# Performance work log

Measured on AMD Instinct MI355X. Metric: run time of the kernel, lower is better.

## Reference

```python
import jax, jax.numpy as jnp
import numpy as np

TAU = 2.0
V_TH = 0.5
SG_ALPHA = 4.0
BN_EPS = 1e-5
NUM_HEADS = 8

@jax.custom_vjp
def spike_fn(x):
    return (x >= 0.0).astype(x.dtype)

def _spike_fwd(x):
    return (x >= 0.0).astype(x.dtype), x

def _spike_bwd(x, g):
    s = jax.nn.sigmoid(SG_ALPHA * x)
    return (g * SG_ALPHA * s * (1.0 - s),)

spike_fn.defvjp(_spike_fwd, _spike_bwd)

def lif(x_seq):
    """Multi-step LIF (spikingjelly step_mode='m'): x_seq [T, ...] -> spikes [T, ...].
    v <- v + (x - v)/tau ; spike = H(v - v_th) ; hard reset with detached spike."""
    def step(v, x):
        v = v + (x - v) / TAU
        s = spike_fn(v - V_TH)
        v = v * (1.0 - jax.lax.stop_gradient(s))
        return v, s
    _, s_seq = jax.lax.scan(step, jnp.zeros_like(x_seq[0]), x_seq)
    return s_seq

def conv1x1(x, w, b=None):
    # x: [T,B,C,H,W], w: [Cout,Cin]
    y = jnp.einsum('tbchw,oc->tbohw', x, w)
    if b is not None:
        y = y + b[:, None, None]
    return y

def bn(x, p):
    # eval-mode BatchNorm2d; p = [gamma, beta, mean, var] each [C]
    g, b, m, v = p[0], p[1], p[2], p[3]
    scale = g / jnp.sqrt(v + BN_EPS)
    return x * scale[:, None, None] + (b - m * scale)[:, None, None]

def setup_inputs() -> dict:
    key = jax.random.key(0)
    ks = jax.random.split(key, 20)
    T, B, C, H, W = 4, 8, 512, 32, 32
    Ch = 2048
    def bn_params(k, c):
        kk = jax.random.split(k, 4)
        gamma = jax.random.uniform(kk[0], (c,), jnp.float32, 0.5, 1.5)
        beta = jax.random.normal(kk[1], (c,), jnp.float32) * 0.1
        mean = jax.random.normal(kk[2], (c,), jnp.float32) * 0.1
        var = jax.random.uniform(kk[3], (c,), jnp.float32, 0.5, 1.5)
        return jnp.stack([gamma, beta, mean, var])
    s = 1.0 / np.sqrt(C)
    sh = 1.0 / np.sqrt(Ch)
    return {
        'x': jax.random.normal(ks[0], (T, B, C, H, W), jnp.float32),
        'q_w': jax.random.normal(ks[1], (C, C), jnp.float32) * s,
        'q_bn': bn_params(ks[2], C),
        'k_w': jax.random.normal(ks[3], (C, C), jnp.float32) * s,
        'k_bn': bn_params(ks[4], C),
        'v_w': jax.random.normal(ks[5], (C, C), jnp.float32) * s,
        'v_bn': bn_params(ks[6], C),
        'th_w': jax.random.normal(ks[7], (NUM_HEADS, NUM_HEADS), jnp.float32) / np.sqrt(NUM_HEADS),
        'proj_w': jax.random.normal(ks[8], (C, C), jnp.float32) * s,
        'proj_b': jax.random.normal(ks[9], (C,), jnp.float32) * 0.02,
        'proj_bn': bn_params(ks[10], C),
        'fc1_w': jax.random.normal(ks[11], (Ch, C), jnp.float32) * s,
        'fc1_b': jax.random.normal(ks[12], (Ch,), jnp.float32) * 0.02,
        'fc1_bn': bn_params(ks[13], Ch),
        'fc2_w': jax.random.normal(ks[14], (C, Ch), jnp.float32) * sh,
        'fc2_b': jax.random.normal(ks[15], (C,), jnp.float32) * 0.02,
        'fc2_bn': bn_params(ks[16], C),
    }

def reference(x, q_w, q_bn, k_w, k_bn, v_w, v_bn, th_w, proj_w, proj_b, proj_bn,
              fc1_w, fc1_b, fc1_bn, fc2_w, fc2_b, fc2_bn):
    T, B, C, H, W = x.shape
    N = H * W
    h = NUM_HEADS
    d = C // h

    # ---- MS_SSA_Conv ----
    identity = x
    xs = lif(x)  # shortcut_lif

    def to_heads(t):  # [T,B,C,H,W] -> [T,B,h,N,d]
        t = t.reshape(T, B, C, N).transpose(0, 1, 3, 2)        # [T,B,N,C]
        return t.reshape(T, B, N, h, d).transpose(0, 1, 3, 2, 4)

    q = to_heads(lif(bn(conv1x1(xs, q_w), q_bn)))
    k = to_heads(lif(bn(conv1x1(xs, k_w), k_bn)))
    v = to_heads(lif(bn(conv1x1(xs, v_w), v_bn)))

    kv = (k * v).sum(axis=3, keepdims=True)                    # [T,B,h,1,d]
    kv = jnp.einsum('tbhod,gh->tbgod', kv, th_w)               # talking heads (Conv1d k=1)
    kv = lif(kv)                                               # talking_heads_lif

    x_att = q * kv                                             # [T,B,h,N,d]
    x_att = x_att.transpose(0, 1, 2, 4, 3).reshape(T, B, C, H, W)
    x_out = bn(conv1x1(x_att, proj_w, proj_b), proj_bn) + identity

    # ---- MS_MLP_Conv (res=False since hidden != in) ----
    identity2 = x_out
    hdn = lif(bn(conv1x1(x_out, fc1_w, fc1_b), fc1_bn))
    out = lif(bn(conv1x1(hdn, fc2_w, fc2_b), fc2_bn)) + identity2
    return out
```

## Files before the change

### kernel.cpp

```cpp
#include <hip/hip_runtime.h>

typedef unsigned char u8;
typedef unsigned int u32;

#define T_STEPS 4
#define B_SZ 8
#define C_IN 512
#define CH 2048
#define N_SP 1024
#define S_C ((size_t)B_SZ * C_IN * N_SP)

__global__ __launch_bounds__(256) void lif_x_kernel(const float* __restrict__ in,
                                                    u8* __restrict__ out)
{
    size_t i = (size_t)blockIdx.x * 256 + threadIdx.x;
    float v = 0.0f;
    #pragma unroll
    for (int t = 0; t < T_STEPS; ++t) {
        float x = in[(size_t)t * S_C + i];
        v += (x - v) * 0.5f;
        u8 s = (v >= 0.5f) ? 1 : 0;
        out[(size_t)t * S_C + i] = s;
        v = s ? 0.0f : v;
    }
}

template<int MODE, int BSRC, bool BIAS, int K, int CO, int NSEL>
__global__ __launch_bounds__(256) void mm(
    const float* __restrict__ W0, const float* __restrict__ W1, const float* __restrict__ W2,
    const void* __restrict__ Xv,
    const float* __restrict__ bn0, const float* __restrict__ bn1, const float* __restrict__ bn2,
    const float* __restrict__ bias,
    const float* __restrict__ kvsf,
    const float* __restrict__ res,
    void* Y0, void* Y1, void* Y2)
{
    constexpr int NB_CO = CO / 64;
    constexpr int NB_N = N_SP / 64;
    constexpr int KT = K / 16;

    __shared__ float As[16][68];
    __shared__ float Xs[4][16][68];

    const int bid = blockIdx.x;
    const int nblk = bid % NB_N;
    int slot = bid / NB_N;
    const int cb = slot % NB_CO; slot /= NB_CO;
    const int sel = (NSEL > 1) ? (slot % NSEL) : 0;
    const int b   = (NSEL > 1) ? (slot / NSEL) : slot;

    const float* W   = (NSEL == 1 || sel == 0) ? W0  : (sel == 1 ? W1  : W2);
    const float* bnp = (NSEL == 1 || sel == 0) ? bn0 : (sel == 1 ? bn1 : bn2);
    void* Yv         = (NSEL == 1 || sel == 0) ? Y0  : (sel == 1 ? Y1  : Y2);

    const int coBase = cb * 64;
    const int n0blk = nblk * 64;
    const int tid = threadIdx.x;
    const int tx = tid & 15, ty = tid >> 4;

    const int wr = tid >> 2;
    const int wk4 = (tid & 3) * 4;

    float scale[4], shift[4];
    #pragma unroll
    for (int i = 0; i < 4; ++i) {
        const int co = coBase + ty * 4 + i;
        const float g = bnp[co], be = bnp[CO + co];
        const float mn = bnp[2 * CO + co], vr = bnp[3 * CO + co];
        scale[i] = g / sqrtf(vr + 1e-5f);
        shift[i] = be - mn * scale[i];
        if (BIAS) shift[i] += bias[co] * scale[i];
    }

    float acc[4][4][4];
    #pragma unroll
    for (int t = 0; t < 4; ++t)
        #pragma unroll
        for (int i = 0; i < 4; ++i)
            #pragma unroll
            for (int j = 0; j < 4; ++j) acc[t][i][j] = 0.0f;

    float4 wreg;
    u32 xu[4];
    float mreg[4];
    float4 xf[4];

    auto prefetch = [&](int kt) {
        wreg = *reinterpret_cast<const float4*>(
            W + (size_t)(coBase + wr) * K + kt * 16 + wk4);
        #pragma unroll
        for (int t = 0; t < 4; ++t) {
            const int tb = t * B_SZ + b;
            if constexpr (BSRC <= 1) {
                xu[t] = *reinterpret_cast<const u32*>(
                    (const u8*)Xv + (size_t)tb * K * N_SP
                    + (size_t)(kt * 16 + ty) * N_SP + n0blk + tx * 4);
                if constexpr (BSRC == 1)
                    mreg[t] = kvsf[(size_t)tb * K + kt * 16 + ty];
            } else {
                xf[t] = *reinterpret_cast<const float4*>(
                    (const float*)Xv + (size_t)tb * K * N_SP
                    + (size_t)(kt * 16 + ty) * N_SP + n0blk + tx * 4);
            }
        }
    };

    prefetch(0);

    for (int kt = 0; kt < KT; ++kt) {
        __syncthreads();
        As[wk4 + 0][wr] = wreg.x;
        As[wk4 + 1][wr] = wreg.y;
        As[wk4 + 2][wr] = wreg.z;
        As[wk4 + 3][wr] = wreg.w;
        #pragma unroll
        for (int t = 0; t < 4; ++t) {
            float4 s0;
            if constexpr (BSRC <= 1) {
                s0.x = (float)( xu[t]        & 0xFFu);
                s0.y = (float)((xu[t] >> 8 ) & 0xFFu);
                s0.z = (float)((xu[t] >> 16) & 0xFFu);
                s0.w = (float)( xu[t] >> 24        );
                if constexpr (BSRC == 1) {
                    s0.x *= mreg[t]; s0.y *= mreg[t];
                    s0.z *= mreg[t]; s0.w *= mreg[t];
                }
            } else {
                s0 = xf[t];
            }
            *reinterpret_cast<float4*>(&Xs[t][ty][tx * 4]) = s0;
        }
        __syncthreads();
        if (kt + 1 < KT) prefetch(kt + 1);

        #pragma unroll
        for (int kk = 0; kk < 16; ++kk) {
            float4 av = *reinterpret_cast<const float4*>(&As[kk][ty * 4]);
            float wa[4] = {av.x, av.y, av.z, av.w};
            #pragma unroll
            for (int t = 0; t < 4; ++t) {
                float4 xv = *reinterpret_cast<const float4*>(&Xs[t][kk][tx * 4]);
                float xw[4] = {xv.x, xv.y, xv.z, xv.w};
                #pragma unroll
                for (int i = 0; i < 4; ++i)
                    #pragma unroll
                    for (int j = 0; j < 4; ++j)
                        acc[t][i][j] += wa[i] * xw[j];
            }
        }
    }

    #pragma unroll
    for (int i = 0; i < 4; ++i) {
        const int co = coBase + ty * 4 + i;
        float v[4] = {0.0f, 0.0f, 0.0f, 0.0f};
        #pragma unroll
        for (int t = 0; t < 4; ++t) {
            const int tb = t * B_SZ + b;
            const size_t off = ((size_t)tb * CO + co) * N_SP + n0blk + tx * 4;
            if constexpr (MODE == 0) {
                u32 pk = 0;
                #pragma unroll
                for (int e = 0; e < 4; ++e) {
                    const float y = acc[t][i][e] * scale[i] + shift[i];
                    v[e] += (y - v[e]) * 0.5f;
                    const u32 s = (v[e] >= 0.5f) ? 1u : 0u;
                    v[e] = s ? 0.0f : v[e];
                    pk |= s << (8 * e);
                }
                *reinterpret_cast<u32*>((u8*)Yv + off) = pk;
            } else if constexpr (MODE == 1) {
                float4 r0 = *reinterpret_cast<const float4*>(res + off);
                float rr[4] = {r0.x, r0.y, r0.z, r0.w};
                float o[4];
                #pragma unroll
                for (int e = 0; e < 4; ++e)
                    o[e] = acc[t][i][e] * scale[i] + shift[i] + rr[e];
                float4 s0 = {o[0], o[1], o[2], o[3]};
                *reinterpret_cast<float4*>((float*)Yv + off) = s0;
            } else {
                float* op = (float*)Yv + off;
                float4 r0 = *reinterpret_cast<const float4*>(op);
                float rr[4] = {r0.x, r0.y, r0.z, r0.w};
                float o[4];
                #pragma unroll
                for (int e = 0; e < 4; ++e) {
                    const float y = acc[t][i][e] * scale[i] + shift[i];
                    v[e] += (y - v[e]) * 0.5f;
                    const u32 s = (v[e] >= 0.5f) ? 1u : 0u;
                    v[e] = s ? 0.0f : v[e];
                    o[e] = rr[e] + (s ? 1.0f : 0.0f);
                }
                float4 s0 = {o[0], o[1], o[2], o[3]};
                *reinterpret_cast<float4*>(op) = s0;
            }
        }
    }
}

__global__ __launch_bounds__(256) void kv_reduce(const u8* __restrict__ ks,
                                                 const u8* __restrict__ vs,
                                                 float* __restrict__ kv)
{
    const int row = blockIdx.x * 4 + (threadIdx.x >> 6);
    const int lane = threadIdx.x & 63;
    const u8* kp = ks + (size_t)row * N_SP;
    const u8* vp = vs + (size_t)row * N_SP;
    int acc = 0;
    #pragma unroll
    for (int n = 0; n < N_SP; n += 256) {
        uchar4 a = *reinterpret_cast<const uchar4*>(kp + n + lane * 4);
        uchar4 c = *reinterpret_cast<const uchar4*>(vp + n + lane * 4);
        acc += (a.x & c.x) + (a.y & c.y) + (a.z & c.z) + (a.w & c.w);
    }
    #pragma unroll
    for (int off = 32; off; off >>= 1) acc += __shfl_down(acc, off, 64);
    if (lane == 0) kv[row] = (float)acc;
}

__global__ __launch_bounds__(256) void th_lif(const float* __restrict__ kvraw,
                                              const float* __restrict__ th,
                                              float* __restrict__ kvs)
{
    const int i = blockIdx.x * 256 + threadIdx.x;
    const int b = i >> 9;
    const int c = i & 511;
    const int g = c >> 6;
    const int dd = c & 63;
    float v = 0.0f;
    #pragma unroll
    for (int t = 0; t < T_STEPS; ++t) {
        const float* base = kvraw + ((size_t)t * B_SZ + b) * C_IN;
        float x = 0.0f;
        #pragma unroll
        for (int hh = 0; hh < 8; ++hh)
            x += base[hh * 64 + dd] * th[g * 8 + hh];
        v += (x - v) * 0.5f;
        const float s = (v >= 0.5f) ? 1.0f : 0.0f;
        kvs[((size_t)t * B_SZ + b) * C_IN + c] = s;
        v = (s != 0.0f) ? 0.0f : v;
    }
}

extern "C" void kernel_launch(void* const* d_in, const int* in_sizes, int n_in,
                              void* d_out, int out_size, void* d_ws, size_t ws_size,
                              hipStream_t stream)
{
    const float* x       = (const float*)d_in[0];
    const float* q_w     = (const float*)d_in[1];
    const float* q_bn    = (const float*)d_in[2];
    const float* k_w     = (const float*)d_in[3];
    const float* k_bn    = (const float*)d_in[4];
    const float* v_w     = (const float*)d_in[5];
    const float* v_bn    = (const float*)d_in[6];
    const float* th_w    = (const float*)d_in[7];
    const float* proj_w  = (const float*)d_in[8];
    const float* proj_b  = (const float*)d_in[9];
    const float* proj_bn = (const float*)d_in[10];
    const float* fc1_w   = (const float*)d_in[11];
    const float* fc1_b   = (const float*)d_in[12];
    const float* fc1_bn  = (const float*)d_in[13];
    const float* fc2_w   = (const float*)d_in[14];
    const float* fc2_b   = (const float*)d_in[15];
    const float* fc2_bn  = (const float*)d_in[16];
    float* out = (float*)d_out;

    u8* ws = (u8*)d_ws;
    const size_t SLOT = (size_t)T_STEPS * S_C;
    u8* xs = ws;
    u8* qs = ws + SLOT;
    u8* ks = ws + 2 * SLOT;
    u8* vs = ws + 3 * SLOT;
    float* kvraw = (float*)(ws + 4 * SLOT);
    float* kvsf  = kvraw + (size_t)T_STEPS * B_SZ * C_IN;
    u8* hdn = ws;

    lif_x_kernel<<<(int)(S_C / 256), 256, 0, stream>>>(x, xs);

    mm<0, 0, false, 512, 512, 3><<<3072, 256, 0, stream>>>(
        q_w, k_w, v_w, xs, q_bn, k_bn, v_bn, nullptr, nullptr, nullptr, qs, ks, vs);

    kv_reduce<<<(T_STEPS * B_SZ * C_IN) / 4, 256, 0, stream>>>(ks, vs, kvraw);
    th_lif<<<(B_SZ * C_IN) / 256, 256, 0, stream>>>(kvraw, th_w, kvsf);

    mm<1, 1, true, 512, 512, 1><<<1024, 256, 0, stream>>>(
        proj_w, nullptr, nullptr, qs, proj_bn, nullptr, nullptr, proj_b, kvsf, x,
        out, nullptr, nullptr);

    mm<0, 2, true, 512, 2048, 1><<<4096, 256, 0, stream>>>(
        fc1_w, nullptr, nullptr, out, fc1_bn, nullptr, nullptr, fc1_b, nullptr, nullptr,
        hdn, nullptr, nullptr);

    mm<2, 0, true, 2048, 512, 1><<<1024, 256, 0, stream>>>(
        fc2_w, nullptr, nullptr, hdn, fc2_bn, nullptr, nullptr, fc2_b, nullptr, nullptr,
        out, nullptr, nullptr);
}
```

Measured before the change: 2.390 ms.

## Parameterize matmul tile height by wave count and reorder block indexing

```diff
diff --git a/kernel.cpp b/kernel.cpp
--- a/kernel.cpp
+++ b/kernel.cpp
@@ -25,8 +25,8 @@
     }
 }
 
-template<int MODE, int BSRC, bool BIAS, int K, int CO, int NSEL>
-__global__ __launch_bounds__(256) void mm(
+template<int NW, int MODE, int BSRC, bool BIAS, int K, int CO, int NSEL>
+__global__ __launch_bounds__(NW * 64) void mm(
     const float* __restrict__ W0, const float* __restrict__ W1, const float* __restrict__ W2,
     const void* __restrict__ Xv,
     const float* __restrict__ bn0, const float* __restrict__ bn1, const float* __restrict__ bn2,
@@ -35,25 +35,29 @@
     const float* __restrict__ res,
     void* Y0, void* Y1, void* Y2)
 {
-    constexpr int NB_CO = CO / 64;
-    constexpr int NB_N = N_SP / 64;
+    constexpr int BM = NW * 16;
+    constexpr int NB_CB = CO / BM;
+    constexpr int CBTOT = NB_CB * NSEL;
     constexpr int KT = K / 16;
-
-    __shared__ float As[16][68];
+    constexpr int TYN = NW * 4;
+    constexpr int HX = 16 / TYN;
+
+    __shared__ float As[16][BM + 4];
     __shared__ float Xs[4][16][68];
 
     const int bid = blockIdx.x;
-    const int nblk = bid % NB_N;
-    int slot = bid / NB_N;
-    const int cb = slot % NB_CO; slot /= NB_CO;
-    const int sel = (NSEL > 1) ? (slot % NSEL) : 0;
-    const int b   = (NSEL > 1) ? (slot / NSEL) : slot;
+    const int cbsel = bid % CBTOT;
+    const int rr = bid / CBTOT;
+    const int nblk = rr % 16;
+    const int b = rr / 16;
+    const int cb = (NSEL > 1) ? (cbsel % NB_CB) : cbsel;
+    const int sel = (NSEL > 1) ? (cbsel / NB_CB) : 0;
 
     const float* W   = (NSEL == 1 || sel == 0) ? W0  : (sel == 1 ? W1  : W2);
     const float* bnp = (NSEL == 1 || sel == 0) ? bn0 : (sel == 1 ? bn1 : bn2);
     void* Yv         = (NSEL == 1 || sel == 0) ? Y0  : (sel == 1 ? Y1  : Y2);
 
-    const int coBase = cb * 64;
+    const int coBase = cb * BM;
     const int n0blk = nblk * 64;
     const int tid = threadIdx.x;
     const int tx = tid & 15, ty = tid >> 4;
@@ -81,9 +85,9 @@
             for (int j = 0; j < 4; ++j) acc[t][i][j] = 0.0f;
 
     float4 wreg;
-    u32 xu[4];
-    float mreg[4];
-    float4 xf[4];
+    u32 xu[4][HX];
+    float mreg[4][HX];
+    float4 xf[4][HX];
 
     auto prefetch = [&](int kt) {
         wreg = *reinterpret_cast<const float4*>(
@@ -91,16 +95,20 @@
         #pragma unroll
         for (int t = 0; t < 4; ++t) {
             const int tb = t * B_SZ + b;
-            if constexpr (BSRC <= 1) {
-                xu[t] = *reinterpret_cast<const u32*>(
-                    (const u8*)Xv + (size_t)tb * K * N_SP
-                    + (size_t)(kt * 16 + ty) * N_SP + n0blk + tx * 4);
-                if constexpr (BSRC == 1)
-                    mreg[t] = kvsf[(size_t)tb * K + kt * 16 + ty];
-            } else {
-                xf[t] = *reinterpret_cast<const float4*>(
-                    (const float*)Xv + (size_t)tb * K * N_SP
-                    + (size_t)(kt * 16 + ty) * N_SP + n0blk + tx * 4);
+            #pragma unroll
+            for (int h = 0; h < HX; ++h) {
+                const int row = kt * 16 + ty + TYN * h;
+                if constexpr (BSRC <= 1) {
+                    xu[t][h] = *reinterpret_cast<const u32*>(
+                        (const u8*)Xv + (size_t)tb * K * N_SP
+                        + (size_t)row * N_SP + n0blk + tx * 4);
+                    if constexpr (BSRC == 1)
+                        mreg[t][h] = kvsf[(size_t)tb * K + row];
+                } else {
+                    xf[t][h] = *reinterpret_cast<const float4*>(
+                        (const float*)Xv + (size_t)tb * K * N_SP
+                        + (size_t)row * N_SP + n0blk + tx * 4);
+                }
             }
         }
     };
@@ -115,20 +123,23 @@
         As[wk4 + 3][wr] = wreg.w;
         #pragma unroll
         for (int t = 0; t < 4; ++t) {
-            float4 s0;
-            if constexpr (BSRC <= 1) {
-                s0.x = (float)( xu[t]        & 0xFFu);
-                s0.y = (float)((xu[t] >> 8 ) & 0xFFu);
-                s0.z = (float)((xu[t] >> 16) & 0xFFu);
-                s0.w = (float)( xu[t] >> 24        );
-                if constexpr (BSRC == 1) {
-                    s0.x *= mreg[t]; s0.y *= mreg[t];
-                    s0.z *= mreg[t]; s0.w *= mreg[t];
+            #pragma unroll
+            for (int h = 0; h < HX; ++h) {
+                float4 s0;
+                if constexpr (BSRC <= 1) {
+                    s0.x = (float)( xu[t][h]        & 0xFFu);
+                    s0.y = (float)((xu[t][h] >> 8 ) & 0xFFu);
+                    s0.z = (float)((xu[t][h] >> 16) & 0xFFu);
+                    s0.w = (float)( xu[t][h] >> 24        );
+                    if constexpr (BSRC == 1) {
+                        s0.x *= mreg[t][h]; s0.y *= mreg[t][h];
+                        s0.z *= mreg[t][h]; s0.w *= mreg[t][h];
+                    }
+                } else {
+                    s0 = xf[t][h];
                 }
-            } else {
-                s0 = xf[t];
+                *reinterpret_cast<float4*>(&Xs[t][ty + TYN * h][tx * 4]) = s0;
             }
-            *reinterpret_cast<float4*>(&Xs[t][ty][tx * 4]) = s0;
         }
         __syncthreads();
         if (kt + 1 < KT) prefetch(kt + 1);
@@ -171,17 +182,17 @@
                 *reinterpret_cast<u32*>((u8*)Yv + off) = pk;
             } else if constexpr (MODE == 1) {
                 float4 r0 = *reinterpret_cast<const float4*>(res + off);
-                float rr[4] = {r0.x, r0.y, r0.z, r0.w};
+                float rr2[4] = {r0.x, r0.y, r0.z, r0.w};
                 float o[4];
                 #pragma unroll
                 for (int e = 0; e < 4; ++e)
-                    o[e] = acc[t][i][e] * scale[i] + shift[i] + rr[e];
+                    o[e] = acc[t][i][e] * scale[i] + shift[i] + rr2[e];
                 float4 s0 = {o[0], o[1], o[2], o[3]};
                 *reinterpret_cast<float4*>((float*)Yv + off) = s0;
             } else {
                 float* op = (float*)Yv + off;
                 float4 r0 = *reinterpret_cast<const float4*>(op);
-                float rr[4] = {r0.x, r0.y, r0.z, r0.w};
+                float rr2[4] = {r0.x, r0.y, r0.z, r0.w};
                 float o[4];
                 #pragma unroll
                 for (int e = 0; e < 4; ++e) {
@@ -189,7 +200,7 @@
                     v[e] += (y - v[e]) * 0.5f;
                     const u32 s = (v[e] >= 0.5f) ? 1u : 0u;
                     v[e] = s ? 0.0f : v[e];
-                    o[e] = rr[e] + (s ? 1.0f : 0.0f);
+                    o[e] = rr2[e] + (s ? 1.0f : 0.0f);
                 }
                 float4 s0 = {o[0], o[1], o[2], o[3]};
                 *reinterpret_cast<float4*>(op) = s0;
@@ -277,21 +288,21 @@
 
     lif_x_kernel<<<(int)(S_C / 256), 256, 0, stream>>>(x, xs);
 
-    mm<0, 0, false, 512, 512, 3><<<3072, 256, 0, stream>>>(
+    mm<2, 0, 0, false, 512, 512, 3><<<6144, 128, 0, stream>>>(
         q_w, k_w, v_w, xs, q_bn, k_bn, v_bn, nullptr, nullptr, nullptr, qs, ks, vs);
 
     kv_reduce<<<(T_STEPS * B_SZ * C_IN) / 4, 256, 0, stream>>>(ks, vs, kvraw);
     th_lif<<<(B_SZ * C_IN) / 256, 256, 0, stream>>>(kvraw, th_w, kvsf);
 
-    mm<1, 1, true, 512, 512, 1><<<1024, 256, 0, stream>>>(
+    mm<2, 1, 1, true, 512, 512, 1><<<2048, 128, 0, stream>>>(
         proj_w, nullptr, nullptr, qs, proj_bn, nullptr, nullptr, proj_b, kvsf, x,
         out, nullptr, nullptr);
 
-    mm<0, 2, true, 512, 2048, 1><<<4096, 256, 0, stream>>>(
+    mm<4, 0, 2, true, 512, 2048, 1><<<4096, 256, 0, stream>>>(
         fc1_w, nullptr, nullptr, out, fc1_bn, nullptr, nullptr, fc1_b, nullptr, nullptr,
         hdn, nullptr, nullptr);
 
-    mm<2, 0, true, 2048, 512, 1><<<1024, 256, 0, stream>>>(
+    mm<2, 2, 0, true, 2048, 512, 1><<<2048, 128, 0, stream>>>(
         fc2_w, nullptr, nullptr, hdn, fc2_bn, nullptr, nullptr, fc2_b, nullptr, nullptr,
         out, nullptr, nullptr);
 }
```

Result: slower. 2.624 ms (+9.8%).

## Retile conv GEMM to 128 output channels by 32 positions with co-major block order

Applied to the files above, without the earlier changes.

```diff
diff --git a/kernel.cpp b/kernel.cpp
--- a/kernel.cpp
+++ b/kernel.cpp
@@ -1,6 +1,7 @@
 #include <hip/hip_runtime.h>
 
 typedef unsigned char u8;
+typedef unsigned short u16;
 typedef unsigned int u32;
 
 #define T_STEPS 4
@@ -35,36 +36,42 @@
     const float* __restrict__ res,
     void* Y0, void* Y1, void* Y2)
 {
-    constexpr int NB_CO = CO / 64;
-    constexpr int NB_N = N_SP / 64;
+    constexpr int NB_CB = CO / 128;
+    constexpr int CBTOT = NB_CB * NSEL;
     constexpr int KT = K / 16;
 
-    __shared__ float As[16][68];
-    __shared__ float Xs[4][16][68];
+    __shared__ float As[16][132];
+    __shared__ float Xs[4][16][36];
 
     const int bid = blockIdx.x;
-    const int nblk = bid % NB_N;
-    int slot = bid / NB_N;
-    const int cb = slot % NB_CO; slot /= NB_CO;
-    const int sel = (NSEL > 1) ? (slot % NSEL) : 0;
-    const int b   = (NSEL > 1) ? (slot / NSEL) : slot;
+    const int cbsel = bid % CBTOT;
+    const int rr = bid / CBTOT;
+    const int nblk = rr & 31;
+    const int b = rr >> 5;
+    const int cb = (NSEL > 1) ? (cbsel % NB_CB) : cbsel;
+    const int sel = (NSEL > 1) ? (cbsel / NB_CB) : 0;
 
     const float* W   = (NSEL == 1 || sel == 0) ? W0  : (sel == 1 ? W1  : W2);
     const float* bnp = (NSEL == 1 || sel == 0) ? bn0 : (sel == 1 ? bn1 : bn2);
     void* Yv         = (NSEL == 1 || sel == 0) ? Y0  : (sel == 1 ? Y1  : Y2);
 
-    const int coBase = cb * 64;
-    const int n0blk = nblk * 64;
+    const int coBase = cb * 128;
+    const int n0blk = nblk * 32;
     const int tid = threadIdx.x;
-    const int tx = tid & 15, ty = tid >> 4;
-
-    const int wr = tid >> 2;
-    const int wk4 = (tid & 3) * 4;
-
-    float scale[4], shift[4];
-    #pragma unroll
-    for (int i = 0; i < 4; ++i) {
-        const int co = coBase + ty * 4 + i;
+    const int tx = tid & 15;
+    const int ty = tid >> 4;
+
+    const int wr = tid >> 1;
+    const int wk8 = (tid & 1) * 8;
+    const int wv = tid >> 6;
+    const int lane = tid & 63;
+    const int xrow = lane >> 2;
+    const int xn0 = (lane & 3) * 8;
+
+    float scale[8], shift[8];
+    #pragma unroll
+    for (int i = 0; i < 8; ++i) {
+        const int co = coBase + ty * 8 + i;
         const float g = bnp[co], be = bnp[CO + co];
         const float mn = bnp[2 * CO + co], vr = bnp[3 * CO + co];
         scale[i] = g / sqrtf(vr + 1e-5f);
@@ -72,127 +79,134 @@
         if (BIAS) shift[i] += bias[co] * scale[i];
     }
 
-    float acc[4][4][4];
+    float acc[4][8][2];
     #pragma unroll
     for (int t = 0; t < 4; ++t)
         #pragma unroll
-        for (int i = 0; i < 4; ++i)
+        for (int i = 0; i < 8; ++i)
             #pragma unroll
-            for (int j = 0; j < 4; ++j) acc[t][i][j] = 0.0f;
-
-    float4 wreg;
-    u32 xu[4];
-    float mreg[4];
-    float4 xf[4];
+            for (int j = 0; j < 2; ++j) acc[t][i][j] = 0.0f;
+
+    const int tbw = wv * B_SZ + b;
+
+    float4 wreg0, wreg1;
+    u32 xa = 0, xb = 0;
+    float mreg = 1.0f;
+    float4 xfa, xfb;
 
     auto prefetch = [&](int kt) {
-        wreg = *reinterpret_cast<const float4*>(
-            W + (size_t)(coBase + wr) * K + kt * 16 + wk4);
+        const float* wp = W + (size_t)(coBase + wr) * K + kt * 16 + wk8;
+        wreg0 = *reinterpret_cast<const float4*>(wp);
+        wreg1 = *reinterpret_cast<const float4*>(wp + 4);
+        if constexpr (BSRC <= 1) {
+            const u8* xp = (const u8*)Xv + (size_t)tbw * K * N_SP
+                           + (size_t)(kt * 16 + xrow) * N_SP + n0blk + xn0;
+            const uint2 u = *reinterpret_cast<const uint2*>(xp);
+            xa = u.x; xb = u.y;
+            if constexpr (BSRC == 1)
+                mreg = kvsf[(size_t)tbw * K + kt * 16 + xrow];
+        } else {
+            const float* xp = (const float*)Xv + (size_t)tbw * K * N_SP
+                              + (size_t)(kt * 16 + xrow) * N_SP + n0blk + xn0;
+            xfa = *reinterpret_cast<const float4*>(xp);
+            xfb = *reinterpret_cast<const float4*>(xp + 4);
+        }
+    };
+
+    prefetch(0);
+
+    for (int kt = 0; kt < KT; ++kt) {
+        __syncthreads();
+        As[wk8 + 0][wr] = wreg0.x;
+        As[wk8 + 1][wr] = wreg0.y;
+        As[wk8 + 2][wr] = wreg0.z;
+        As[wk8 + 3][wr] = wreg0.w;
+        As[wk8 + 4][wr] = wreg1.x;
+        As[wk8 + 5][wr] = wreg1.y;
+        As[wk8 + 6][wr] = wreg1.z;
+        As[wk8 + 7][wr] = wreg1.w;
+        {
+            float4 s0, s1;
+            if constexpr (BSRC <= 1) {
+                s0.x = (float)( xa        & 0xFFu);
+                s0.y = (float)((xa >> 8 ) & 0xFFu);
+                s0.z = (float)((xa >> 16) & 0xFFu);
+                s0.w = (float)( xa >> 24        );
+                s1.x = (float)( xb        & 0xFFu);
+                s1.y = (float)((xb >> 8 ) & 0xFFu);
+                s1.z = (float)((xb >> 16) & 0xFFu);
+                s1.w = (float)( xb >> 24        );
+                if constexpr (BSRC == 1) {
+                    s0.x *= mreg; s0.y *= mreg; s0.z *= mreg; s0.w *= mreg;
+                    s1.x *= mreg; s1.y *= mreg; s1.z *= mreg; s1.w *= mreg;
+                }
+            } else {
+                s0 = xfa; s1 = xfb;
+            }
+            *reinterpret_cast<float4*>(&Xs[wv][xrow][xn0]) = s0;
+            *reinterpret_cast<float4*>(&Xs[wv][xrow][xn0 + 4]) = s1;
+        }
+        __syncthreads();
+        if (kt + 1 < KT) prefetch(kt + 1);
+
+        #pragma unroll
+        for (int kk = 0; kk < 16; ++kk) {
+            float4 a0 = *reinterpret_cast<const float4*>(&As[kk][ty * 8]);
+            float4 a1 = *reinterpret_cast<const float4*>(&As[kk][ty * 8 + 4]);
+            float wa[8] = {a0.x, a0.y, a0.z, a0.w, a1.x, a1.y, a1.z, a1.w};
+            #pragma unroll
+            for (int t = 0; t < 4; ++t) {
+                float2 xv = *reinterpret_cast<const float2*>(&Xs[t][kk][tx * 2]);
+                float xw[2] = {xv.x, xv.y};
+                #pragma unroll
+                for (int i = 0; i < 8; ++i)
+                    #pragma unroll
+                    for (int j = 0; j < 2; ++j)
+                        acc[t][i][j] += wa[i] * xw[j];
+            }
+        }
+    }
+
+    #pragma unroll
+    for (int i = 0; i < 8; ++i) {
+        const int co = coBase + ty * 8 + i;
+        float v[2] = {0.0f, 0.0f};
         #pragma unroll
         for (int t = 0; t < 4; ++t) {
             const int tb = t * B_SZ + b;
-            if constexpr (BSRC <= 1) {
-                xu[t] = *reinterpret_cast<const u32*>(
-                    (const u8*)Xv + (size_t)tb * K * N_SP
-                    + (size_t)(kt * 16 + ty) * N_SP + n0blk + tx * 4);
-                if constexpr (BSRC == 1)
-                    mreg[t] = kvsf[(size_t)tb * K + kt * 16 + ty];
-            } else {
-                xf[t] = *reinterpret_cast<const float4*>(
-                    (const float*)Xv + (size_t)tb * K * N_SP
-                    + (size_t)(kt * 16 + ty) * N_SP + n0blk + tx * 4);
-            }
-        }
-    };
-
-    prefetch(0);
-
-    for (int kt = 0; kt < KT; ++kt) {
-        __syncthreads();
-        As[wk4 + 0][wr] = wreg.x;
-        As[wk4 + 1][wr] = wreg.y;
-        As[wk4 + 2][wr] = wreg.z;
-        As[wk4 + 3][wr] = wreg.w;
-        #pragma unroll
-        for (int t = 0; t < 4; ++t) {
-            float4 s0;
-            if constexpr (BSRC <= 1) {
-                s0.x = (float)( xu[t]        & 0xFFu);
-                s0.y = (float)((xu[t] >> 8 ) & 0xFFu);
-                s0.z = (float)((xu[t] >> 16) & 0xFFu);
-                s0.w = (float)( xu[t] >> 24        );
-                if constexpr (BSRC == 1) {
-                    s0.x *= mreg[t]; s0.y *= mreg[t];
-                    s0.z *= mreg[t]; s0.w *= mreg[t];
-                }
-            } else {
-                s0 = xf[t];
-            }
-            *reinterpret_cast<float4*>(&Xs[t][ty][tx * 4]) = s0;
-        }
-        __syncthreads();
-        if (kt + 1 < KT) prefetch(kt + 1);
-
-        #pragma unroll
-        for (int kk = 0; kk < 16; ++kk) {
-            float4 av = *reinterpret_cast<const float4*>(&As[kk][ty * 4]);
-            float wa[4] = {av.x, av.y, av.z, av.w};
-            #pragma unroll
-            for (int t = 0; t < 4; ++t) {
-                float4 xv = *reinterpret_cast<const float4*>(&Xs[t][kk][tx * 4]);
-                float xw[4] = {xv.x, xv.y, xv.z, xv.w};
-                #pragma unroll
-                for (int i = 0; i < 4; ++i)
-                    #pragma unroll
-                    for (int j = 0; j < 4; ++j)
-                        acc[t][i][j] += wa[i] * xw[j];
-            }
-        }
-    }
-
-    #pragma unroll
-    for (int i = 0; i < 4; ++i) {
-        const int co = coBase + ty * 4 + i;
-        float v[4] = {0.0f, 0.0f, 0.0f, 0.0f};
-        #pragma unroll
-        for (int t = 0; t < 4; ++t) {
-            const int tb = t * B_SZ + b;
-            const size_t off = ((size_t)tb * CO + co) * N_SP + n0blk + tx * 4;
+            const size_t off = ((size_t)tb * CO + co) * N_SP + n0blk + tx * 2;
             if constexpr (MODE == 0) {
                 u32 pk = 0;
                 #pragma unroll
-                for (int e = 0; e < 4; ++e) {
+                for (int e = 0; e < 2; ++e) {
                     const float y = acc[t][i][e] * scale[i] + shift[i];
                     v[e] += (y - v[e]) * 0.5f;
                     const u32 s = (v[e] >= 0.5f) ? 1u : 0u;
                     v[e] = s ? 0.0f : v[e];
                     pk |= s << (8 * e);
                 }
-                *reinterpret_cast<u32*>((u8*)Yv + off) = pk;
+                *reinterpret_cast<u16*>((u8*)Yv + off) = (u16)pk;
             } else if constexpr (MODE == 1) {
-                float4 r0 = *reinterpret_cast<const float4*>(res + off);
-                float rr[4] = {r0.x, r0.y, r0.z, r0.w};
-                float o[4];
-                #pragma unroll
-                for (int e = 0; e < 4; ++e)
-                    o[e] = acc[t][i][e] * scale[i] + shift[i] + rr[e];
-                float4 s0 = {o[0], o[1], o[2], o[3]};
-                *reinterpret_cast<float4*>((float*)Yv + off) = s0;
+                const float2 r0 = *reinterpret_cast<const float2*>(res + off);
+                float2 s0;
+                s0.x = acc[t][i][0] * scale[i] + shift[i] + r0.x;
+                s0.y = acc[t][i][1] * scale[i] + shift[i] + r0.y;
+                *reinterpret_cast<float2*>((float*)Yv + off) = s0;
             } else {
                 float* op = (float*)Yv + off;
-                float4 r0 = *reinterpret_cast<const float4*>(op);
-                float rr[4] = {r0.x, r0.y, r0.z, r0.w};
-                float o[4];
+                const float2 r0 = *reinterpret_cast<const float2*>(op);
+                float rr2[2] = {r0.x, r0.y};
+                float o[2];
                 #pragma unroll
-                for (int e = 0; e < 4; ++e) {
+                for (int e = 0; e < 2; ++e) {
                     const float y = acc[t][i][e] * scale[i] + shift[i];
                     v[e] += (y - v[e]) * 0.5f;
                     const u32 s = (v[e] >= 0.5f) ? 1u : 0u;
                     v[e] = s ? 0.0f : v[e];
-                    o[e] = rr[e] + (s ? 1.0f : 0.0f);
+                    o[e] = rr2[e] + (s ? 1.0f : 0.0f);
                 }
-                float4 s0 = {o[0], o[1], o[2], o[3]};
-                *reinterpret_cast<float4*>(op) = s0;
+                float2 s0 = {o[0], o[1]};
+                *reinterpret_cast<float2*>(op) = s0;
             }
         }
     }
```

Result: slower. 2.494 ms (+4.4%).

## Give each wavefront private LDS tiles and remove block-wide barriers in GEMM

Applied to the files above, without the earlier changes.

```diff
diff --git a/kernel.cpp b/kernel.cpp
--- a/kernel.cpp
+++ b/kernel.cpp
@@ -35,17 +35,16 @@
     const float* __restrict__ res,
     void* Y0, void* Y1, void* Y2)
 {
-    constexpr int NB_CO = CO / 64;
-    constexpr int NB_N = N_SP / 64;
-    constexpr int KT = K / 16;
-
-    __shared__ float As[16][68];
-    __shared__ float Xs[4][16][68];
+    constexpr int NB_CB = CO / 64;
+    constexpr int KT = K / 8;
+
+    __shared__ float Ws[4][8][66];
+    __shared__ float Xs[4][4][8][18];
 
     const int bid = blockIdx.x;
-    const int nblk = bid % NB_N;
-    int slot = bid / NB_N;
-    const int cb = slot % NB_CO; slot /= NB_CO;
+    const int nblk = bid % 16;
+    int slot = bid / 16;
+    const int cb = slot % NB_CB; slot /= NB_CB;
     const int sel = (NSEL > 1) ? (slot % NSEL) : 0;
     const int b   = (NSEL > 1) ? (slot / NSEL) : slot;
 
@@ -54,17 +53,22 @@
     void* Yv         = (NSEL == 1 || sel == 0) ? Y0  : (sel == 1 ? Y1  : Y2);
 
     const int coBase = cb * 64;
-    const int n0blk = nblk * 64;
     const int tid = threadIdx.x;
-    const int tx = tid & 15, ty = tid >> 4;
-
-    const int wr = tid >> 2;
-    const int wk4 = (tid & 3) * 4;
+    const int wv = tid >> 6;
+    const int lane = tid & 63;
+    const int cog = lane >> 2;
+    const int ng = lane & 3;
+    const int nW = nblk * 64 + wv * 16;
+
+    const int xr = lane >> 1;
+    const int xt = xr >> 3;
+    const int xk = xr & 7;
+    const int xseg = (lane & 1) * 8;
 
     float scale[4], shift[4];
     #pragma unroll
     for (int i = 0; i < 4; ++i) {
-        const int co = coBase + ty * 4 + i;
+        const int co = coBase + cog * 4 + i;
         const float g = bnp[co], be = bnp[CO + co];
         const float mn = bnp[2 * CO + co], vr = bnp[3 * CO + co];
         scale[i] = g / sqrtf(vr + 1e-5f);
@@ -80,67 +84,70 @@
             #pragma unroll
             for (int j = 0; j < 4; ++j) acc[t][i][j] = 0.0f;
 
-    float4 wreg;
-    u32 xu[4];
-    float mreg[4];
-    float4 xf[4];
+    const float* wRow = W + (size_t)(coBase + lane) * K;
+    const int tbx = xt * B_SZ + b;
+    const u8* xuBase = (const u8*)Xv + (size_t)tbx * K * N_SP + nW + xseg;
+    const float* xfBase = (const float*)Xv + (size_t)tbx * K * N_SP + nW + xseg;
+
+    float wpre[8];
+    u32 xa = 0, xb = 0;
+    float mreg = 1.0f;
+    float4 xfa, xfb;
 
     auto prefetch = [&](int kt) {
-        wreg = *reinterpret_cast<const float4*>(
-            W + (size_t)(coBase + wr) * K + kt * 16 + wk4);
-        #pragma unroll
-        for (int t = 0; t < 4; ++t) {
-            const int tb = t * B_SZ + b;
-            if constexpr (BSRC <= 1) {
-                xu[t] = *reinterpret_cast<const u32*>(
-                    (const u8*)Xv + (size_t)tb * K * N_SP
-                    + (size_t)(kt * 16 + ty) * N_SP + n0blk + tx * 4);
-                if constexpr (BSRC == 1)
-                    mreg[t] = kvsf[(size_t)tb * K + kt * 16 + ty];
-            } else {
-                xf[t] = *reinterpret_cast<const float4*>(
-                    (const float*)Xv + (size_t)tb * K * N_SP
-                    + (size_t)(kt * 16 + ty) * N_SP + n0blk + tx * 4);
-            }
+        const float* wp = wRow + kt * 8;
+        *reinterpret_cast<float4*>(&wpre[0]) = *reinterpret_cast<const float4*>(wp);
+        *reinterpret_cast<float4*>(&wpre[4]) = *reinterpret_cast<const float4*>(wp + 4);
+        const int krow = kt * 8 + xk;
+        if constexpr (BSRC <= 1) {
+            const uint2 u = *reinterpret_cast<const uint2*>(xuBase + (size_t)krow * N_SP);
+            xa = u.x; xb = u.y;
+            if constexpr (BSRC == 1)
+                mreg = kvsf[(size_t)tbx * K + krow];
+        } else {
+            const float* xp = xfBase + (size_t)krow * N_SP;
+            xfa = *reinterpret_cast<const float4*>(xp);
+            xfb = *reinterpret_cast<const float4*>(xp + 4);
         }
     };
 
     prefetch(0);
 
+    #pragma unroll 1
     for (int kt = 0; kt < KT; ++kt) {
-        __syncthreads();
-        As[wk4 + 0][wr] = wreg.x;
-        As[wk4 + 1][wr] = wreg.y;
-        As[wk4 + 2][wr] = wreg.z;
-        As[wk4 + 3][wr] = wreg.w;
-        #pragma unroll
-        for (int t = 0; t < 4; ++t) {
-            float4 s0;
+        #pragma unroll
+        for (int j = 0; j < 8; ++j) Ws[wv][j][lane] = wpre[j];
+        {
+            float4 s0, s1;
             if constexpr (BSRC <= 1) {
-                s0.x = (float)( xu[t]        & 0xFFu);
-                s0.y = (float)((xu[t] >> 8 ) & 0xFFu);
-                s0.z = (float)((xu[t] >> 16) & 0xFFu);
-                s0.w = (float)( xu[t] >> 24        );
+                s0.x = (float)( xa        & 0xFFu);
+                s0.y = (float)((xa >> 8 ) & 0xFFu);
+                s0.z = (float)((xa >> 16) & 0xFFu);
+                s0.w = (float)( xa >> 24        );
+                s1.x = (float)( xb        & 0xFFu);
+                s1.y = (float)((xb >> 8 ) & 0xFFu);
+                s1.z = (float)((xb >> 16) & 0xFFu);
+                s1.w = (float)( xb >> 24        );
                 if constexpr (BSRC == 1) {
-                    s0.x *= mreg[t]; s0.y *= mreg[t];
-                    s0.z *= mreg[t]; s0.w *= mreg[t];
+                    s0.x *= mreg; s0.y *= mreg; s0.z *= mreg; s0.w *= mreg;
+                    s1.x *= mreg; s1.y *= mreg; s1.z *= mreg; s1.w *= mreg;
                 }
             } else {
-                s0 = xf[t];
+                s0 = xfa; s1 = xfb;
             }
-            *reinterpret_cast<float4*>(&Xs[t][ty][tx * 4]) = s0;
+            *reinterpret_cast<float4*>(&Xs[wv][xt][xk][xseg]) = s0;
+            *reinterpret_cast<float4*>(&Xs[wv][xt][xk][xseg + 4]) = s1;
         }
-        __syncthreads();
         if (kt + 1 < KT) prefetch(kt + 1);
 
         #pragma unroll
-        for (int kk = 0; kk < 16; ++kk) {
-            float4 av = *reinterpret_cast<const float4*>(&As[kk][ty * 4]);
+        for (int kk = 0; kk < 8; ++kk) {
+            float4 av = *reinterpret_cast<const float4*>(&Ws[wv][kk][cog * 4]);
             float wa[4] = {av.x, av.y, av.z, av.w};
             #pragma unroll
             for (int t = 0; t < 4; ++t) {
-                float4 xv = *reinterpret_cast<const float4*>(&Xs[t][kk][tx * 4]);
-                float xw[4] = {xv.x, xv.y, xv.z, xv.w};
+                float4 xq = *reinterpret_cast<const float4*>(&Xs[wv][t][kk][ng * 4]);
+                float xw[4] = {xq.x, xq.y, xq.z, xq.w};
                 #pragma unroll
                 for (int i = 0; i < 4; ++i)
                     #pragma unroll
@@ -152,12 +159,12 @@
 
     #pragma unroll
     for (int i = 0; i < 4; ++i) {
-        const int co = coBase + ty * 4 + i;
+        const int co = coBase + cog * 4 + i;
         float v[4] = {0.0f, 0.0f, 0.0f, 0.0f};
         #pragma unroll
         for (int t = 0; t < 4; ++t) {
             const int tb = t * B_SZ + b;
-            const size_t off = ((size_t)tb * CO + co) * N_SP + n0blk + tx * 4;
+            const size_t off = ((size_t)tb * CO + co) * N_SP + nW + ng * 4;
             if constexpr (MODE == 0) {
                 u32 pk = 0;
                 #pragma unroll
@@ -171,17 +178,17 @@
                 *reinterpret_cast<u32*>((u8*)Yv + off) = pk;
             } else if constexpr (MODE == 1) {
                 float4 r0 = *reinterpret_cast<const float4*>(res + off);
-                float rr[4] = {r0.x, r0.y, r0.z, r0.w};
+                float rr2[4] = {r0.x, r0.y, r0.z, r0.w};
                 float o[4];
                 #pragma unroll
                 for (int e = 0; e < 4; ++e)
-                    o[e] = acc[t][i][e] * scale[i] + shift[i] + rr[e];
+                    o[e] = acc[t][i][e] * scale[i] + shift[i] + rr2[e];
                 float4 s0 = {o[0], o[1], o[2], o[3]};
                 *reinterpret_cast<float4*>((float*)Yv + off) = s0;
             } else {
                 float* op = (float*)Yv + off;
                 float4 r0 = *reinterpret_cast<const float4*>(op);
-                float rr[4] = {r0.x, r0.y, r0.z, r0.w};
+                float rr2[4] = {r0.x, r0.y, r0.z, r0.w};
                 float o[4];
                 #pragma unroll
                 for (int e = 0; e < 4; ++e) {
@@ -189,7 +196,7 @@
                     v[e] += (y - v[e]) * 0.5f;
                     const u32 s = (v[e] >= 0.5f) ? 1u : 0u;
                     v[e] = s ? 0.0f : v[e];
-                    o[e] = rr[e] + (s ? 1.0f : 0.0f);
+                    o[e] = rr2[e] + (s ? 1.0f : 0.0f);
                 }
                 float4 s0 = {o[0], o[1], o[2], o[3]};
                 *reinterpret_cast<float4*>(op) = s0;
```

After: 2.453 ms, median of 2. 1.03x slower.
